# Kernel tuning notes

Measured on AMD Instinct MI355X. Metric: run time of the kernel, lower is better.

Reference implementation:

```python
import jax, jax.numpy as jnp
import numpy as np

N_MSB = 4
WB = 8       # weight bits
ABNM = 8     # activation bits for non-MVM ops
NL = 0.1     # noise level
B, IN, H = 256, 1024, 1024


def pact_a(x, a):
    # sign(x) * 0.5 * (|x| - ||x|-a| + a)  == sign(x)*min(|x|, a) for a>0
    return jnp.sign(x) * 0.5 * (jnp.abs(x) - jnp.abs(jnp.abs(x) - a) + a)


def _quant_val(x, bits, x_range):
    step = 2.0 ** (bits - 1)
    x01 = jnp.clip(x / x_range, -1.0 + 1.0 / step, 1.0 - 1.0 / step)
    return jnp.round(x01 * step) / step * x_range


def quant_ste(x, bits, x_range):
    # QuantFunc: straight-through estimator (identity grad wrt x, none wrt range)
    return x + jax.lax.stop_gradient(_quant_val(x, bits, x_range) - x)


def bitsplit(x, n_msb):
    # x in [0,1] -> n_msb binary planes stacked on axis 0, plus beta coefficients
    l1 = 2.0 ** n_msb - 1.0
    ys, betas = [], []
    for i in range(n_msb):
        l2 = 2.0 ** (n_msb - (i + 1))
        betas.append(l2 / l1)
        ys.append(jnp.mod(jnp.floor(jnp.round(l1 * x) / l2), 2.0))
    return jnp.stack(ys), jnp.asarray(betas, dtype=x.dtype)


def noisy_qmm(x, w, b, eps_w, eps_b):
    # CustomMM_bmm: quantized weights + gaussian noise in fwd; STE-style bwd.
    w_eff = w + jax.lax.stop_gradient(_quant_val(w, WB, 1.0) - w + eps_w * jnp.max(w) * NL)
    b_eff = b + jax.lax.stop_gradient(_quant_val(b, WB, 1.0) - b + eps_b * jnp.max(b) * NL)
    return jnp.einsum('nbi,nio->nbo', x, w_eff) + b_eff  # [n_msb, B, 4H]


def lstm_cell_q_bs(input, hx, cx, weight_ih, weight_hh, bias_ih, bias_hh,
                   eps_w_ih, eps_w_hh, eps_b_ih, eps_b_hh,
                   a1, a3, a4, a5, a6, a7, a8, a9, a10, a11):
    inp01 = (pact_a(input, a1) + a1) / (a1 * 2.0)            # [B, IN] in [0,1]
    inp_msb, beta = bitsplit(inp01, N_MSB)                   # [n_msb,B,IN], [n_msb]
    o1 = noisy_qmm(inp_msb, weight_ih, bias_ih, eps_w_ih, eps_b_ih)
    o2 = noisy_qmm(inp_msb, weight_hh, bias_hh, eps_w_hh, eps_b_hh)
    out = (o1 > 0.5).astype(inp01.dtype) + (o2 > 0.5).astype(inp01.dtype)
    gates = jnp.einsum('n,nbo->bo', beta, out)               # part1; part2 undefined in source -> 0
    i, j, f, o = jnp.split(gates, 4, axis=1)                 # each [B, H]
    forget_gate_out = quant_ste(pact_a(jax.nn.sigmoid(f), a3), ABNM, a3)
    input_gate_out = quant_ste(pact_a(jax.nn.sigmoid(i), a4), ABNM, a4)
    activation_out = quant_ste(pact_a(jnp.tanh(j), a5), ABNM, a5)
    output_gate_out = quant_ste(pact_a(jax.nn.sigmoid(o), a6), ABNM, a6)
    gated_cell = quant_ste(pact_a(cx * forget_gate_out, a7), ABNM, a7)
    activated_input = quant_ste(pact_a(input_gate_out * activation_out, a8), ABNM, a8)
    new_c = quant_ste(pact_a(gated_cell + activated_input, a9), ABNM, a9)
    activated_cell = quant_ste(pact_a(jnp.tanh(new_c), a10), ABNM, a10)
    new_h = quant_ste(pact_a(activated_cell * output_gate_out, a11), ABNM, a11)
    return new_h, new_c


def setup_inputs() -> dict:
    key = jax.random.key(0)
    ks = jax.random.split(key, 12)
    d = {
        'input': jax.random.normal(ks[0], (B, IN), jnp.float32),
        'hx': jax.random.normal(ks[1], (B, H), jnp.float32),
        'cx': jax.random.normal(ks[2], (B, H), jnp.float32),
        'weight_ih': jax.random.normal(ks[3], (N_MSB, IN, 4 * H), jnp.float32),
        'weight_hh': jax.random.normal(ks[4], (N_MSB, IN, 4 * H), jnp.float32),
        'bias_ih': jax.random.normal(ks[5], (N_MSB, 1, 4 * H), jnp.float32),
        'bias_hh': jax.random.normal(ks[6], (N_MSB, 1, 4 * H), jnp.float32),
        'eps_w_ih': jax.random.normal(ks[7], (N_MSB, IN, 4 * H), jnp.float32),
        'eps_w_hh': jax.random.normal(ks[8], (N_MSB, IN, 4 * H), jnp.float32),
        'eps_b_ih': jax.random.normal(ks[9], (N_MSB, 1, 4 * H), jnp.float32),
        'eps_b_hh': jax.random.normal(ks[10], (N_MSB, 1, 4 * H), jnp.float32),
    }
    a_init = {'a1': 128.0, 'a3': 1.0, 'a4': 1.0, 'a5': 1.0, 'a6': 1.0,
              'a7': 4.0, 'a8': 1.0, 'a9': 4.0, 'a10': 1.0, 'a11': 4.0}
    for name, v in a_init.items():
        d[name] = jnp.array([v], jnp.float32)
    return d


def reference(input, hx, cx, weight_ih, weight_hh, bias_ih, bias_hh,
              eps_w_ih, eps_w_hh, eps_b_ih, eps_b_hh,
              a1, a3, a4, a5, a6, a7, a8, a9, a10, a11):
    return lstm_cell_q_bs(input, hx, cx, weight_ih, weight_hh, bias_ih, bias_hh,
                          eps_w_ih, eps_w_hh, eps_b_ih, eps_b_hh,
                          a1, a3, a4, a5, a6, a7, a8, a9, a10, a11)
```

## Files before the change

### kernel.cpp

```cpp
#include <hip/hip_runtime.h>
#include <hip/hip_bf16.h>
#include <math.h>

typedef int   v4i __attribute__((ext_vector_type(4)));
typedef float v4f __attribute__((ext_vector_type(4)));

#define B_DIM   256
#define IN_DIM  1024
#define H4      4096
#define NPLANE  4
#define WELEM   (NPLANE * IN_DIM * H4)
#define XELEM   (B_DIM * IN_DIM)

#define WS_X_OFF      (64 + 262144)
#define WS_CMP_OFF    (64 + 262144 + 1048576)

__global__ void k_max(const float* __restrict__ wih, const float* __restrict__ whh,
                      const float* __restrict__ bih, const float* __restrict__ bhh,
                      float* __restrict__ outm) {
  int b = blockIdx.x, t = threadIdx.x;
  const float* src; long n4; int slot; long bb, nb;
  if (b < 512)       { src = wih; n4 = WELEM / 4; slot = 0; bb = b;       nb = 512; }
  else if (b < 1024) { src = whh; n4 = WELEM / 4; slot = 1; bb = b - 512; nb = 512; }
  else if (b == 1024){ src = bih; n4 = 16384 / 4; slot = 2; bb = 0;       nb = 1;   }
  else               { src = bhh; n4 = 16384 / 4; slot = 3; bb = 0;       nb = 1;   }
  const v4f* p = (const v4f*)src;
  float m = -3.4e38f;
  for (long i = bb * 256 + t; i < n4; i += nb * 256) {
    v4f v = p[i];
    m = fmaxf(m, fmaxf(fmaxf(v.x, v.y), fmaxf(v.z, v.w)));
  }
#pragma unroll
  for (int off = 32; off >= 1; off >>= 1) m = fmaxf(m, __shfl_down(m, off, 64));
  __shared__ float sm[4];
  int w = t >> 6, ln = t & 63;
  if (ln == 0) sm[w] = m;
  __syncthreads();
  if (t == 0) {
    m = fmaxf(fmaxf(sm[0], sm[1]), fmaxf(sm[2], sm[3]));
    atomicMax((int*)&outm[slot], __float_as_int(m));
  }
}

__global__ void k_prep(const float* __restrict__ input, const float* __restrict__ a1p,
                       signed char* __restrict__ X) {
  int gid = blockIdx.x * 256 + threadIdx.x;
  float a1 = a1p[0];
  float x = input[gid];
  float t = fabsf(x), u = fabsf(t - a1);
  float sg = (x > 0.f) ? 0.5f : ((x < 0.f) ? -0.5f : 0.f);
  float p = sg * ((t - u) + a1);
  float inp01 = (p + a1) / (a1 * 2.0f);
  float q = rintf(15.0f * inp01);
  int qi = (int)q;
#pragma unroll
  for (int pl = 0; pl < 4; ++pl)
    X[pl * XELEM + gid] = (signed char)((qi >> (3 - pl)) & 1);
}

__global__ __launch_bounds__(512, 4) void k_gemm(
    const float* __restrict__ Wih, const float* __restrict__ Whh,
    const float* __restrict__ Eih, const float* __restrict__ Ehh,
    const float* __restrict__ bih, const float* __restrict__ bhh,
    const float* __restrict__ ebih, const float* __restrict__ ebhh,
    const float* __restrict__ maxm,
    const signed char* __restrict__ X, unsigned char* __restrict__ cmp) {
  const int ntile = blockIdx.x;
  const int sp = blockIdx.y;
  const int s = sp >> 2, plane = sp & 3;
  const float* W = s ? Whh : Wih;
  const float* E = s ? Ehh : Eih;
  const float maxw = maxm[s];

  const int tid = threadIdx.x;
  const int wave = tid >> 6, lane = tid & 63, quad = lane >> 4, l15 = lane & 15;

  __shared__ __align__(16) unsigned char Blds[2 * 4 * 32 * 64];

  const int sn = tid & 31;
  const int kq = tid >> 5;
  const int k0 = kq << 2;
  const int wr_off = sn * 64 + ((((kq >> 2) ^ ((sn >> 1) & 3)) << 4) | ((kq & 3) << 2));

  v4i acc[4][2][2];
#pragma unroll
  for (int d = 0; d < 4; ++d)
#pragma unroll
    for (int m = 0; m < 2; ++m)
#pragma unroll
      for (int n = 0; n < 2; ++n) acc[d][m][n] = (v4i){0, 0, 0, 0};

  const float* wp = W + (size_t)(plane * IN_DIM + k0) * H4 + (size_t)ntile * 32 + sn;
  const float* ep = E + (size_t)(plane * IN_DIM + k0) * H4 + (size_t)ntile * 32 + sn;

  const signed char* Xp = X + plane * XELEM;
  const int arow0 = wave * 32 + l15;

  auto digitize_write = [&](const float wv[4], const float evv[4], int bf) {
    unsigned int pk0 = 0, pk1 = 0, pk2 = 0, pk3 = 0;
#pragma unroll
    for (int j = 0; j < 4; ++j) {
      float w = wv[j], ev = evv[j];
      float xc = fminf(fmaxf(w, -0.9921875f), 0.9921875f);
      float qv = rintf(xc * 128.f) * 0.0078125f;
      float noise = (ev * maxw) * 0.1f;
      float a = w + ((qv - w) + noise);
      float x0 = a * 8.f;    float f0 = rintf(x0); float r0 = x0 - f0;
      float x1 = r0 * 128.f; float f1 = rintf(x1); float r1 = x1 - f1;
      float x2 = r1 * 128.f; float f2 = rintf(x2); float r2 = x2 - f2;
      float x3 = r2 * 128.f; float f3 = rintf(x3);
      pk0 |= ((unsigned int)((int)f0 & 255)) << (8 * j);
      pk1 |= ((unsigned int)((int)f1 & 255)) << (8 * j);
      pk2 |= ((unsigned int)((int)f2 & 255)) << (8 * j);
      pk3 |= ((unsigned int)((int)f3 & 255)) << (8 * j);
    }
    unsigned char* base = Blds + bf * 8192 + wr_off;
    *(unsigned int*)(base)        = pk0;
    *(unsigned int*)(base + 2048) = pk1;
    *(unsigned int*)(base + 4096) = pk2;
    *(unsigned int*)(base + 6144) = pk3;
  };

  {
    float w4[4], e4[4];
#pragma unroll
    for (int j = 0; j < 4; ++j) { w4[j] = wp[(size_t)j * H4]; e4[j] = ep[(size_t)j * H4]; }
    digitize_write(w4, e4, 0);
  }
  v4i afr[2];
  afr[0] = *(const v4i*)(Xp + (arow0) * IN_DIM + quad * 16);
  afr[1] = *(const v4i*)(Xp + (arow0 + 16) * IN_DIM + quad * 16);
  __syncthreads();

  for (int ch = 0; ch < 16; ++ch) {
    const int buf = ch & 1;
    float nw[4], ne[4];
    v4i anx[2]; anx[0] = afr[0]; anx[1] = afr[1];
    if (ch < 15) {
      size_t off = (size_t)(ch + 1) * 64 * H4;
#pragma unroll
      for (int j = 0; j < 4; ++j) { nw[j] = wp[off + (size_t)j * H4]; ne[j] = ep[off + (size_t)j * H4]; }
      anx[0] = *(const v4i*)(Xp + (arow0) * IN_DIM + (ch + 1) * 64 + quad * 16);
      anx[1] = *(const v4i*)(Xp + (arow0 + 16) * IN_DIM + (ch + 1) * 64 + quad * 16);
    }
    const unsigned char* rb = Blds + buf * 8192;
#pragma unroll
    for (int d = 0; d < 4; ++d) {
#pragma unroll
      for (int ns = 0; ns < 2; ++ns) {
        const int nr = ns * 16 + l15;
        v4i bfr = *(const v4i*)(rb + d * 2048 + nr * 64 + ((quad ^ ((nr >> 1) & 3)) << 4));
        acc[d][0][ns] = __builtin_amdgcn_mfma_i32_16x16x64_i8(afr[0], bfr, acc[d][0][ns], 0, 0, 0);
        acc[d][1][ns] = __builtin_amdgcn_mfma_i32_16x16x64_i8(afr[1], bfr, acc[d][1][ns], 0, 0, 0);
      }
    }
    if (ch < 15) digitize_write(nw, ne, buf ^ 1);
    afr[0] = anx[0]; afr[1] = anx[1];
    __syncthreads();
  }

  const float* bp  = s ? bhh : bih;
  const float* ebp = s ? ebhh : ebih;
  const float mb = maxm[2 + s];
  const double inv = 1.0 / 16777216.0;
  unsigned char* cp = cmp + (size_t)sp * B_DIM * H4;
#pragma unroll
  for (int ns = 0; ns < 2; ++ns) {
    int col = ntile * 32 + ns * 16 + l15;
    float bv = bp[plane * H4 + col], ev = ebp[plane * H4 + col];
    float xc = fminf(fmaxf(bv, -0.9921875f), 0.9921875f);
    float qv = rintf(xc * 128.f) * 0.0078125f;
    float noise = (ev * mb) * 0.1f;
    float beff = bv + ((qv - bv) + noise);
    double th = 0.5 - (double)beff;
#pragma unroll
    for (int ms = 0; ms < 2; ++ms) {
#pragma unroll
      for (int r = 0; r < 4; ++r) {
        long long T = ((long long)acc[0][ms][ns][r] << 21) + ((long long)acc[1][ms][ns][r] << 14)
                    + ((long long)acc[2][ms][ns][r] << 7)  +  (long long)acc[3][ms][ns][r];
        int row = wave * 32 + ms * 16 + quad * 4 + r;
        cp[(size_t)row * H4 + col] = ((double)T * inv > th) ? 1 : 0;
      }
    }
  }
}

__device__ __forceinline__ float pact_(float x, float a) {
  float t = fabsf(x), u = fabsf(t - a);
  float sg = (x > 0.f) ? 0.5f : ((x < 0.f) ? -0.5f : 0.f);
  return sg * ((t - u) + a);
}
__device__ __forceinline__ float quant_(float x, float a) {
  float xr = x / a;
  xr = fminf(fmaxf(xr, -0.9921875f), 0.9921875f);
  return rintf(xr * 128.f) * 0.0078125f * a;
}
__device__ __forceinline__ float sigm_(float x) { return 1.0f / (1.0f + expf(-x)); }

__global__ void k_pointwise(const unsigned char* __restrict__ cmp, const float* __restrict__ cx,
                            const float* a3, const float* a4, const float* a5, const float* a6,
                            const float* a7, const float* a8, const float* a9, const float* a10,
                            const float* a11, float* __restrict__ out) {
  int idx = blockIdx.x * 256 + threadIdx.x;
  int b = idx >> 10, h = idx & 1023;
  float g[4];
#pragma unroll
  for (int gi = 0; gi < 4; ++gi) {
    int col = gi * 1024 + h;
    float acc = 0.f;
#pragma unroll
    for (int n = 0; n < 4; ++n) {
      int o = (int)cmp[((size_t)(0 * 4 + n) * B_DIM + b) * H4 + col]
            + (int)cmp[((size_t)(1 * 4 + n) * B_DIM + b) * H4 + col];
      float beta = (float)(8 >> n) / 15.0f;
      acc = acc + beta * (float)o;
    }
    g[gi] = acc;
  }
  float fg = quant_(pact_(sigm_(g[2]), a3[0]), a3[0]);
  float ig = quant_(pact_(sigm_(g[0]), a4[0]), a4[0]);
  float ac = quant_(pact_(tanhf(g[1]), a5[0]), a5[0]);
  float og = quant_(pact_(sigm_(g[3]), a6[0]), a6[0]);
  float cxv = cx[idx];
  float gc = quant_(pact_(cxv * fg, a7[0]), a7[0]);
  float ai = quant_(pact_(ig * ac, a8[0]), a8[0]);
  float nc = quant_(pact_(gc + ai, a9[0]), a9[0]);
  float acl = quant_(pact_(tanhf(nc), a10[0]), a10[0]);
  float nh = quant_(pact_(acl * og, a11[0]), a11[0]);
  out[idx] = nh;
  out[XELEM + idx] = nc;
}

extern "C" void kernel_launch(void* const* d_in, const int* in_sizes, int n_in,
                              void* d_out, int out_size, void* d_ws, size_t ws_size,
                              hipStream_t stream) {
  (void)in_sizes; (void)n_in; (void)out_size; (void)ws_size;
  const float* input = (const float*)d_in[0];
  const float* cx    = (const float*)d_in[2];
  const float* wih   = (const float*)d_in[3];
  const float* whh   = (const float*)d_in[4];
  const float* bih   = (const float*)d_in[5];
  const float* bhh   = (const float*)d_in[6];
  const float* ewih  = (const float*)d_in[7];
  const float* ewhh  = (const float*)d_in[8];
  const float* ebih  = (const float*)d_in[9];
  const float* ebhh  = (const float*)d_in[10];
  const float* a1    = (const float*)d_in[11];
  const float* a3    = (const float*)d_in[12];
  const float* a4    = (const float*)d_in[13];
  const float* a5    = (const float*)d_in[14];
  const float* a6    = (const float*)d_in[15];
  const float* a7    = (const float*)d_in[16];
  const float* a8    = (const float*)d_in[17];
  const float* a9    = (const float*)d_in[18];
  const float* a10   = (const float*)d_in[19];
  const float* a11   = (const float*)d_in[20];
  float* out = (float*)d_out;

  char* ws = (char*)d_ws;
  float*         maxm = (float*)ws;
  signed char*   X    = (signed char*)(ws + WS_X_OFF);
  unsigned char* cmp  = (unsigned char*)(ws + WS_CMP_OFF);

  hipMemsetAsync(ws, 0, 64, stream);
  k_max<<<1026, 256, 0, stream>>>(wih, whh, bih, bhh, maxm);
  k_prep<<<1024, 256, 0, stream>>>(input, a1, X);
  k_gemm<<<dim3(128, 8), 512, 0, stream>>>(wih, whh, ewih, ewhh, bih, bhh, ebih, ebhh,
                                           maxm, X, cmp);
  k_pointwise<<<1024, 256, 0, stream>>>(cmp, cx, a3, a4, a5, a6, a7, a8, a9, a10, a11, out);
}
```

Baseline: 347.1 us.

## Vectorize weight/noise loads and transpose packed bytes via cross-lane shuffles

Each thread now loads four consecutive columns of W and E as float4 vectors instead of four strided scalar rows. A lane shuffle and byte-permute transpose rebuilds the k-major packed int8 layout that LDS expects. Global weight prefetch is deepened to two chunks ahead, and launch bounds drop to 2 waves per SIMD so the extra registers fit. The aim is fewer, wider global memory transactions and more latency hiding, at the cost of shuffle ALU work and possibly lower occupancy.

After: 341.6 us. Within noise of the previous version (-1.6%).

```diff
diff --git a/kernel.cpp b/kernel.cpp
--- a/kernel.cpp
+++ b/kernel.cpp
@@ -58,7 +58,7 @@
     X[pl * XELEM + gid] = (signed char)((qi >> (3 - pl)) & 1);
 }
 
-__global__ __launch_bounds__(512, 4) void k_gemm(
+__global__ __launch_bounds__(512, 2) void k_gemm(
     const float* __restrict__ Wih, const float* __restrict__ Whh,
     const float* __restrict__ Eih, const float* __restrict__ Ehh,
     const float* __restrict__ bih, const float* __restrict__ bhh,
@@ -77,10 +77,15 @@
 
   __shared__ __align__(16) unsigned char Blds[2 * 4 * 32 * 64];
 
-  const int sn = tid & 31;
-  const int kq = tid >> 5;
-  const int k0 = kq << 2;
-  const int wr_off = sn * 64 + ((((kq >> 2) ^ ((sn >> 1) & 3)) << 4) | ((kq & 3) << 2));
+  const int kl  = tid >> 3;
+  const int nc4 = (tid & 7) << 2;
+  const int p  = (lane >> 3) & 3;
+  const int sq = p & 1, qq = p >> 1;
+  const unsigned sel1 = sq ? 0x03070206u : 0x05010400u;
+  const unsigned sel2 = qq ? 0x03020706u : 0x05040100u;
+  const int snW = nc4 + 2 * sq + qq;
+  const int kqW = (wave << 1) + (lane >> 5);
+  const int wr_off = snW * 64 + ((((kqW >> 2) ^ ((snW >> 1) & 3)) << 4) | ((kqW & 3) << 2));
 
   v4i acc[4][2][2];
 #pragma unroll
@@ -90,17 +95,18 @@
 #pragma unroll
       for (int n = 0; n < 2; ++n) acc[d][m][n] = (v4i){0, 0, 0, 0};
 
-  const float* wp = W + (size_t)(plane * IN_DIM + k0) * H4 + (size_t)ntile * 32 + sn;
-  const float* ep = E + (size_t)(plane * IN_DIM + k0) * H4 + (size_t)ntile * 32 + sn;
+  const size_t cstep = (size_t)64 * H4;
+  const float* wp = W + ((size_t)plane * IN_DIM + kl) * H4 + (size_t)ntile * 32 + nc4;
+  const float* ep = E + ((size_t)plane * IN_DIM + kl) * H4 + (size_t)ntile * 32 + nc4;
 
   const signed char* Xp = X + plane * XELEM;
   const int arow0 = wave * 32 + l15;
 
-  auto digitize_write = [&](const float wv[4], const float evv[4], int bf) {
-    unsigned int pk0 = 0, pk1 = 0, pk2 = 0, pk3 = 0;
+  auto digitize4 = [&](v4f w4, v4f e4, unsigned pk[4]) {
+    pk[0] = pk[1] = pk[2] = pk[3] = 0;
 #pragma unroll
     for (int j = 0; j < 4; ++j) {
-      float w = wv[j], ev = evv[j];
+      float w = w4[j], ev = e4[j];
       float xc = fminf(fmaxf(w, -0.9921875f), 0.9921875f);
       float qv = rintf(xc * 128.f) * 0.0078125f;
       float noise = (ev * maxw) * 0.1f;
@@ -109,24 +115,34 @@
       float x1 = r0 * 128.f; float f1 = rintf(x1); float r1 = x1 - f1;
       float x2 = r1 * 128.f; float f2 = rintf(x2); float r2 = x2 - f2;
       float x3 = r2 * 128.f; float f3 = rintf(x3);
-      pk0 |= ((unsigned int)((int)f0 & 255)) << (8 * j);
-      pk1 |= ((unsigned int)((int)f1 & 255)) << (8 * j);
-      pk2 |= ((unsigned int)((int)f2 & 255)) << (8 * j);
-      pk3 |= ((unsigned int)((int)f3 & 255)) << (8 * j);
-    }
+      pk[0] |= ((unsigned)((int)f0 & 255)) << (8 * j);
+      pk[1] |= ((unsigned)((int)f1 & 255)) << (8 * j);
+      pk[2] |= ((unsigned)((int)f2 & 255)) << (8 * j);
+      pk[3] |= ((unsigned)((int)f3 & 255)) << (8 * j);
+    }
+  };
+  auto transpose_write = [&](const unsigned pk[4], int bf) {
     unsigned char* base = Blds + bf * 8192 + wr_off;
-    *(unsigned int*)(base)        = pk0;
-    *(unsigned int*)(base + 2048) = pk1;
-    *(unsigned int*)(base + 4096) = pk2;
-    *(unsigned int*)(base + 6144) = pk3;
+#pragma unroll
+    for (int d = 0; d < 4; ++d) {
+      unsigned A = pk[d];
+      unsigned t = (unsigned)__shfl_xor((int)A, 8, 64);
+      unsigned D = __builtin_amdgcn_perm(t, A, sel1);
+      unsigned Ex = (unsigned)__shfl_xor((int)D, 16, 64);
+      unsigned o = __builtin_amdgcn_perm(Ex, D, sel2);
+      *(unsigned*)(base + d * 2048) = o;
+    }
   };
 
+  unsigned pk[4];
   {
-    float w4[4], e4[4];
-#pragma unroll
-    for (int j = 0; j < 4; ++j) { w4[j] = wp[(size_t)j * H4]; e4[j] = ep[(size_t)j * H4]; }
-    digitize_write(w4, e4, 0);
-  }
+    v4f w4 = *(const v4f*)wp;
+    v4f e4 = *(const v4f*)ep;
+    digitize4(w4, e4, pk);
+    transpose_write(pk, 0);
+  }
+  v4f wA = *(const v4f*)(wp + cstep);
+  v4f eA = *(const v4f*)(ep + cstep);
   v4i afr[2];
   afr[0] = *(const v4i*)(Xp + (arow0) * IN_DIM + quad * 16);
   afr[1] = *(const v4i*)(Xp + (arow0 + 16) * IN_DIM + quad * 16);
@@ -134,14 +150,15 @@
 
   for (int ch = 0; ch < 16; ++ch) {
     const int buf = ch & 1;
-    float nw[4], ne[4];
-    v4i anx[2]; anx[0] = afr[0]; anx[1] = afr[1];
+    v4f wB = wA, eB = eA;
+    v4i anx0 = afr[0], anx1 = afr[1];
+    if (ch < 14) {
+      wB = *(const v4f*)(wp + (size_t)(ch + 2) * cstep);
+      eB = *(const v4f*)(ep + (size_t)(ch + 2) * cstep);
+    }
     if (ch < 15) {
-      size_t off = (size_t)(ch + 1) * 64 * H4;
-#pragma unroll
-      for (int j = 0; j < 4; ++j) { nw[j] = wp[off + (size_t)j * H4]; ne[j] = ep[off + (size_t)j * H4]; }
-      anx[0] = *(const v4i*)(Xp + (arow0) * IN_DIM + (ch + 1) * 64 + quad * 16);
-      anx[1] = *(const v4i*)(Xp + (arow0 + 16) * IN_DIM + (ch + 1) * 64 + quad * 16);
+      anx0 = *(const v4i*)(Xp + (arow0) * IN_DIM + (ch + 1) * 64 + quad * 16);
+      anx1 = *(const v4i*)(Xp + (arow0 + 16) * IN_DIM + (ch + 1) * 64 + quad * 16);
     }
     const unsigned char* rb = Blds + buf * 8192;
 #pragma unroll
@@ -154,8 +171,12 @@
         acc[d][1][ns] = __builtin_amdgcn_mfma_i32_16x16x64_i8(afr[1], bfr, acc[d][1][ns], 0, 0, 0);
       }
     }
-    if (ch < 15) digitize_write(nw, ne, buf ^ 1);
-    afr[0] = anx[0]; afr[1] = anx[1];
+    if (ch < 15) {
+      digitize4(wA, eA, pk);
+      transpose_write(pk, buf ^ 1);
+      wA = wB; eA = eB;
+    }
+    afr[0] = anx0; afr[1] = anx1;
     __syncthreads();
   }
 
```
